# Kernel tuning notes

Hardware: AMD Instinct MI355X
Metric: run time of the kernel (lower is better)

The kernel has to match this reference:

```python
import jax, jax.numpy as jnp
import numpy as np
from jax import lax

B, C, L = 64, 768, 197
DEG = 3          # KACN Chebyshev degree
KW = 3           # conv kernel size
EPS = 1e-5       # BatchNorm eps
END_X = 14.0     # RoPE grid width (14x14 patch grid + 1 CLS token)


def _conv1d(x, W):
    # x: (B, Cin, L), W: (Cout, Cin, K); padding=1 keeps length
    return lax.conv_general_dilated(x, W, window_strides=(1,), padding=[(1, 1)],
                                    dimension_numbers=('NCH', 'OIH', 'NCH'))


def _batchnorm(y, scale, bias):
    # training-mode BatchNorm1d: biased stats over (batch, length)
    mean = jnp.mean(y, axis=(0, 2), keepdims=True)
    var = jnp.var(y, axis=(0, 2), keepdims=True)
    return (y - mean) * lax.rsqrt(var + EPS) * scale[None, :, None] + bias[None, :, None]


def _kacn_proj(x, W, scale, bias):
    # KACNConv1DLayer (groups=1): cos(arange(deg+1) * arccos(tanh(x))) basis, conv, BN
    b, c, l = x.shape
    z = jnp.arccos(jnp.tanh(x))[:, :, None, :] * jnp.arange(DEG + 1, dtype=x.dtype)[None, None, :, None]
    z = jnp.cos(z).reshape(b, c * (DEG + 1), l)  # (B, C*(DEG+1), L), channel-major pairing
    return _batchnorm(_conv1d(z, W), scale, bias)


def _rope(t, cosang, sinang):
    # rotate consecutive channel pairs; t: (B, N, C), cos/sin: (N, C//2)
    b, n, c = t.shape
    p = t.reshape(b, n, c // 2, 2)
    a, bb = p[..., 0], p[..., 1]
    ra = a * cosang[None] - bb * sinang[None]
    rb = a * sinang[None] + bb * cosang[None]
    return jnp.stack([ra, rb], axis=-1).reshape(b, n, c)


def reference(x, Wq, Wk, Wv, bnq_s, bnq_b, bnk_s, bnk_b, bnv_s, bnv_b, gamma, freqs, norm_s, norm_b):
    q = _kacn_proj(x, Wq, bnq_s, bnq_b)
    k = _kacn_proj(x, Wk, bnk_s, bnk_b)
    v = _kacn_proj(x, Wv, bnv_s, bnv_b)
    b, c, l = v.shape
    Q = q.transpose(0, 2, 1)  # (B, L, C)
    K = k.transpose(0, 2, 1)
    # mixed 2D RoPE angles (num_heads=1): t_x, t_y over 14x14 grid
    t = jnp.arange(l - 1, dtype=x.dtype)
    tx = jnp.mod(t, END_X)
    ty = jnp.floor(t / END_X)
    ang = tx[:, None] * freqs[0][None, :] + ty[:, None] * freqs[1][None, :]  # (L-1, C//2)
    cosang, sinang = jnp.cos(ang), jnp.sin(ang)
    # token 0 (CLS) is not rotated
    Qr = jnp.concatenate([Q[:, :1], _rope(Q[:, 1:], cosang, sinang)], axis=1)
    Kr = jnp.concatenate([K[:, :1], _rope(K[:, 1:], cosang, sinang)], axis=1)
    energy = jnp.einsum('bic,bjc->bij', Qr, Kr)          # unscaled, as in the module
    att = jax.nn.softmax(energy, axis=-1)
    out = jnp.einsum('bcj,bij->bci', v, att)             # v @ att^T
    return _batchnorm(gamma[0] * x + out, norm_s, norm_b)


def setup_inputs() -> dict:
    key = jax.random.key(0)
    ks = jax.random.split(key, 5)
    std = 1.0 / (C * (DEG + 1) * KW)
    x = jax.random.normal(ks[0], (B, C, L), dtype=jnp.float32)
    Wq = jax.random.normal(ks[1], (C, C * (DEG + 1), KW), dtype=jnp.float32) * std
    Wk = jax.random.normal(ks[2], (C, C * (DEG + 1), KW), dtype=jnp.float32) * std
    Wv = jax.random.normal(ks[3], (C, C * (DEG + 1), KW), dtype=jnp.float32) * std
    ones = jnp.ones((C,), jnp.float32)
    zeros = jnp.zeros((C,), jnp.float32)
    # init_2d_freqs(dim=C, num_heads=1, theta=10, rotate=True).view(2, -1)
    mag = 1.0 / 10.0 ** (np.arange(0, C, 4)[: C // 4].astype(np.float32) / C)
    ang = float(jax.random.uniform(ks[4], ())) * 2.0 * np.pi
    fx = np.concatenate([mag * np.cos(ang), mag * np.cos(np.pi / 2 + ang)])
    fy = np.concatenate([mag * np.sin(ang), mag * np.sin(np.pi / 2 + ang)])
    freqs = jnp.asarray(np.stack([fx, fy], axis=0), dtype=jnp.float32)  # (2, C//2)
    return {"x": x, "Wq": Wq, "Wk": Wk, "Wv": Wv,
            "bnq_s": ones, "bnq_b": zeros, "bnk_s": ones, "bnk_b": zeros,
            "bnv_s": ones, "bnv_b": zeros,
            "gamma": jnp.zeros((1,), jnp.float32), "freqs": freqs,
            "norm_s": ones, "norm_b": zeros}
```

## Files before the change

kernel.cpp:

```cpp
#include <hip/hip_runtime.h>

#define CCH 768
#define LL  197
#define L199 199
#define KC  2304
#define KTOT 6912
#define MK2 1769472
#define NVALID 12736
#define NROW 12608

typedef __bf16 bf16x8 __attribute__((ext_vector_type(8)));
typedef float f32x2 __attribute__((ext_vector_type(2)));
typedef float f32x4 __attribute__((ext_vector_type(4)));
typedef float f32x16 __attribute__((ext_vector_type(16)));

__device__ __forceinline__ unsigned short f2bf(float f) {
  unsigned int u = __float_as_uint(f);
  u += 0x7FFFu + ((u >> 16) & 1u);
  return (unsigned short)(u >> 16);
}
__device__ __forceinline__ float bf2f(unsigned short h) {
  return __uint_as_float(((unsigned int)h) << 16);
}

__global__ void pack_bias(const float* __restrict__ Wq, const float* __restrict__ Wk,
                          const float* __restrict__ Wv, unsigned short* __restrict__ Apack,
                          float* __restrict__ bias3, size_t pack1_halves) {
  __shared__ float wrow[9216];
  __shared__ float red0[256], red1[256], red2[256];
  const int bid = blockIdx.x;
  const int proj = bid / 768, m = bid % 768;
  const int t = threadIdx.x;
  const float* W = proj == 0 ? Wq : (proj == 1 ? Wk : Wv);
  const float* src = W + (size_t)m * 9216;
#pragma unroll
  for (int s = 0; s < 36; ++s) wrow[t + 256 * s] = src[t + 256 * s];
  __syncthreads();
  float s0 = 0.f, s1 = 0.f, s2 = 0.f;
  for (int c = t; c < 768; c += 256) {
    s0 += wrow[12 * c];
    s1 += wrow[12 * c + 1];
    s2 += wrow[12 * c + 2];
  }
  red0[t] = s0; red1[t] = s1; red2[t] = s2;
  unsigned short* Ahi = Apack + (size_t)proj * pack1_halves;
  unsigned short* Alo = Ahi + (size_t)768 * KTOT;
#pragma unroll
  for (int s = 0; s < 9; ++s) {
    int u = t + 256 * s;
    int c = u / 3, dm1 = u % 3;
    int ci = c * 4 + dm1 + 1;
#pragma unroll
    for (int tap = 0; tap < 3; ++tap) {
      float f = wrow[ci * 3 + tap];
      unsigned short hi = f2bf(f);
      unsigned short lo = f2bf(f - bf2f(hi));
      size_t idx = (size_t)m * KTOT + tap * KC + u;
      Ahi[idx] = hi;
      Alo[idx] = lo;
    }
  }
  __syncthreads();
  for (int off = 128; off; off >>= 1) {
    if (t < off) {
      red0[t] += red0[t + off];
      red1[t] += red1[t + off];
      red2[t] += red2[t + off];
    }
    __syncthreads();
  }
  if (t == 0) {
    bias3[proj * 2304 + m] = red0[0];
    bias3[proj * 2304 + 768 + m] = red1[0];
    bias3[proj * 2304 + 1536 + m] = red2[0];
  }
}

__global__ void z_kernel(const float* __restrict__ x, unsigned short* __restrict__ Zhi,
                         unsigned short* __restrict__ Zlo) {
  __shared__ float zs[3][32][33];
  int c0 = blockIdx.x * 32, l0 = blockIdx.y * 32, b = blockIdx.z;
  int t = threadIdx.x;
#pragma unroll
  for (int s = 0; s < 4; ++s) {
    int u = t + 256 * s;
    int rc = u >> 5, cl = u & 31;
    float v = 0.f;
    if (l0 + cl < LL) v = x[((size_t)b * CCH + c0 + rc) * LL + l0 + cl];
    float t1 = tanhf(v);
    zs[0][rc][cl] = t1;
    zs[1][rc][cl] = 2.f * t1 * t1 - 1.f;
    zs[2][rc][cl] = t1 * (4.f * t1 * t1 - 3.f);
  }
  __syncthreads();
#pragma unroll
  for (int s = 0; s < 12; ++s) {
    int w = t + 256 * s;
    int rl = w / 96, cc = w % 96;
    if (l0 + rl < LL) {
      int cl2 = cc / 3, dm1 = cc % 3;
      float v = zs[dm1][cl2][rl];
      unsigned short hi = f2bf(v);
      unsigned short lo = f2bf(v - bf2f(hi));
      size_t row = (size_t)b * L199 + 1 + l0 + rl;
      Zhi[row * KC + c0 * 3 + cc] = hi;
      Zlo[row * KC + c0 * 3 + cc] = lo;
    }
  }
}

__global__ void zero_zpad(unsigned short* __restrict__ Zhi, unsigned short* __restrict__ Zlo) {
  int u = blockIdx.x * 256 + threadIdx.x;
  if (u >= 132 * KC) return;
  int rowi = u / KC, c = u % KC;
  size_t r = (rowi < 128) ? ((size_t)(rowi >> 1) * L199 + (size_t)(rowi & 1) * 198)
                          : ((size_t)NVALID + rowi - 128);
  Zhi[r * KC + c] = 0;
  Zlo[r * KC + c] = 0;
}

#define GLL(SRC, DST) \
  __builtin_amdgcn_global_load_lds( \
      (const __attribute__((address_space(1))) void*)(SRC), \
      (__attribute__((address_space(3))) void*)(DST), 16, 0, 0)

__global__ __launch_bounds__(512, 2) void conv_gemm3(const unsigned short* __restrict__ Apack,
                                                     const unsigned short* __restrict__ Zhi,
                                                     const unsigned short* __restrict__ Zlo,
                                                     const float* __restrict__ bias3,
                                                     float* __restrict__ Oqk,
                                                     float* __restrict__ Ov) {
  __shared__ unsigned short lds[2 * 4 * 8192];
  const int bid = blockIdx.x;
  const int xcd = bid & 7, loc = bid >> 3;
  const int wg = (xcd < 2) ? (xcd * 57 + loc) : (114 + (xcd - 2) * 56 + loc);
  const int n_t = wg / 9, rem = wg % 9;
  const int proj = rem / 3, m_t = rem % 3;
  const int m_blk = m_t * 256, n_blk = n_t * 256;
  const unsigned short* Ahi = Apack + (size_t)proj * 2 * 768 * KTOT;
  const unsigned short* Alo = Ahi + (size_t)768 * KTOT;
  const float* bias3p = bias3 + proj * 2304;
  float* Op = (proj == 2) ? Ov : Oqk + (size_t)proj * NROW * CCH;

  const int t = threadIdx.x;
  const int wave = t >> 6, lane = t & 63;
  const int wm = (wave >> 2) * 128, wn = (wave & 3) * 64;
  f32x16 acc[4][2] = {};

  const int lt = ((lane >> 4) & 1) * 512 + (lane >> 5) * 128 + (lane & 15) * 8;
  const int auoff = (wm >> 4) * 512 + lt;
  const int buoff = (wn >> 4) * 512 + lt;

  const int prow = lane & 15;
  const int kch = lane >> 4;
  const unsigned short* srcs[8];
  int doff[8];
#pragma unroll
  for (int j = 0; j < 8; ++j) {
    int u = (wave << 3) + j;
    int tile = u >> 4, p = u & 15;
    doff[j] = tile * 8192 + p * 512;
    int r;
    const unsigned short* g;
    int rs;
    if (tile < 2) {
      r = m_blk + p * 16 + prow;
      g = (tile == 0) ? Ahi : Alo;
      rs = KTOT;
    } else {
      r = n_blk + p * 16 + prow;
      if (r > 12737) r = 12737;
      g = (tile == 2) ? Zhi : Zlo;
      rs = KC;
    }
    srcs[j] = g + (size_t)r * rs + kch * 8;
  }

  const int NIT = KTOT / 32;
#pragma unroll
  for (int j = 0; j < 8; ++j) GLL(srcs[j], lds + doff[j]);
#pragma unroll
  for (int j = 0; j < 6; ++j) GLL(srcs[j] + 32, lds + 32768 + doff[j]);
  asm volatile("s_waitcnt vmcnt(6)\n\ts_barrier" ::: "memory");
  __builtin_amdgcn_sched_barrier(0);

  for (int i = 0; i < NIT; ++i) {
    const unsigned short* lb = lds + ((i & 1) ? 32768 : 0);
    unsigned short* othbuf = lds + ((i & 1) ? 0 : 32768);
    unsigned short* curbuf = lds + ((i & 1) ? 32768 : 0);
    const int koff_prev = 32 * (i + 1);
    const int koff_cur  = 32 * (i + 2);
    const bool stage_prev = (i < NIT - 1);
    const bool stage_cur  = (i < NIT - 2);

    bf16x8 bh[2][2], bl[2][2];
    bf16x8 ah[2], al[2];

#pragma unroll
    for (int ks = 0; ks < 2; ++ks) {
#pragma unroll
      for (int nb = 0; nb < 2; ++nb) {
        bh[nb][ks] = *(const bf16x8*)(lb + 16384 + buoff + nb * 1024 + ks * 256);
        bl[nb][ks] = *(const bf16x8*)(lb + 24576 + buoff + nb * 1024 + ks * 256);
      }
      ah[ks] = *(const bf16x8*)(lb + auoff + ks * 256);
      al[ks] = *(const bf16x8*)(lb + 8192 + auoff + ks * 256);
    }
    if (stage_prev) {
      GLL(srcs[6] + koff_prev, othbuf + doff[6]);
      GLL(srcs[7] + koff_prev, othbuf + doff[7]);
    }
    asm volatile("s_barrier\n\ts_waitcnt lgkmcnt(0)" ::: "memory");
    __builtin_amdgcn_sched_barrier(0);
    __builtin_amdgcn_s_setprio(1);
#pragma unroll
    for (int p = 0; p < 3; ++p)
#pragma unroll
      for (int ks = 0; ks < 2; ++ks)
#pragma unroll
        for (int nb = 0; nb < 2; ++nb) {
          acc[0][nb] = __builtin_amdgcn_mfma_f32_32x32x16_bf16(
              p == 2 ? al[ks] : ah[ks], p == 1 ? bl[nb][ks] : bh[nb][ks], acc[0][nb], 0, 0, 0);
        }
    __builtin_amdgcn_s_setprio(0);
    asm volatile("s_barrier" ::: "memory");
    __builtin_amdgcn_sched_barrier(0);

#define PHASEQ(Q)                                                                 \
    {                                                                             \
      _Pragma("unroll") for (int ks = 0; ks < 2; ++ks) {                          \
        ah[ks] = *(const bf16x8*)(lb + auoff + (Q) * 1024 + ks * 256);            \
        al[ks] = *(const bf16x8*)(lb + 8192 + auoff + (Q) * 1024 + ks * 256);     \
      }                                                                           \
      if (stage_cur) {                                                            \
        GLL(srcs[2 * ((Q) - 1)] + koff_cur, curbuf + doff[2 * ((Q) - 1)]);        \
        GLL(srcs[2 * ((Q) - 1) + 1] + koff_cur, curbuf + doff[2 * ((Q) - 1) + 1]);\
      }                                                                           \
      asm volatile("s_barrier\n\ts_waitcnt lgkmcnt(0)" ::: "memory");             \
      __builtin_amdgcn_sched_barrier(0);                                          \
      __builtin_amdgcn_s_setprio(1);                                              \
      _Pragma("unroll") for (int p = 0; p < 3; ++p)                               \
      _Pragma("unroll") for (int ks = 0; ks < 2; ++ks)                            \
      _Pragma("unroll") for (int nb = 0; nb < 2; ++nb) {                          \
        acc[Q][nb] = __builtin_amdgcn_mfma_f32_32x32x16_bf16(                     \
            p == 2 ? al[ks] : ah[ks], p == 1 ? bl[nb][ks] : bh[nb][ks],           \
            acc[Q][nb], 0, 0, 0);                                                 \
      }                                                                           \
      __builtin_amdgcn_s_setprio(0);                                              \
    }

    PHASEQ(1)
    asm volatile("s_barrier" ::: "memory");
    __builtin_amdgcn_sched_barrier(0);
    PHASEQ(2)
    asm volatile("s_barrier" ::: "memory");
    __builtin_amdgcn_sched_barrier(0);
    PHASEQ(3)
    if (i < NIT - 2) {
      asm volatile("s_waitcnt vmcnt(6)\n\ts_barrier" ::: "memory");
    } else if (i == NIT - 2) {
      asm volatile("s_waitcnt vmcnt(0)\n\ts_barrier" ::: "memory");
    }
    __builtin_amdgcn_sched_barrier(0);
#undef PHASEQ
  }

  int rowarr[2];
  bool val[2], v0[2], v2[2];
#pragma unroll
  for (int nb = 0; nb < 2; ++nb) {
    int n = n_blk + wn + nb * 32 + (lane & 31);
    int b = n / L199, nl = n - b * L199;
    val[nb] = (n < NVALID) && (nl < LL);
    rowarr[nb] = b * LL + nl;
    v0[nb] = (nl == 0);
    v2[nb] = (nl == 196);
  }
#pragma unroll
  for (int mb = 0; mb < 4; ++mb) {
#pragma unroll
    for (int q = 0; q < 4; ++q) {
      int m = m_blk + wm + mb * 32 + q * 8 + (lane >> 5) * 4;
      f32x4 b0 = *(const f32x4*)(bias3p + m);
      f32x4 b1 = *(const f32x4*)(bias3p + 768 + m);
      f32x4 b2 = *(const f32x4*)(bias3p + 1536 + m);
      f32x4 bs = b0 + b1 + b2;
#pragma unroll
      for (int nb = 0; nb < 2; ++nb) {
        if (val[nb]) {
          f32x4 r;
          r[0] = acc[mb][nb][q * 4 + 0];
          r[1] = acc[mb][nb][q * 4 + 1];
          r[2] = acc[mb][nb][q * 4 + 2];
          r[3] = acc[mb][nb][q * 4 + 3];
          r += bs;
          if (v0[nb]) r -= b0;
          if (v2[nb]) r -= b2;
          *(f32x4*)(Op + (size_t)rowarr[nb] * CCH + m) = r;
        }
      }
    }
  }
}

__global__ void zero_f32(float* __restrict__ p, int n) {
  int u = blockIdx.x * 256 + threadIdx.x;
  if (u < n) p[u] = 0.f;
}

__global__ void bn_stats(const float* __restrict__ Oqk, const float* __restrict__ Ov,
                         float* __restrict__ Ssum, float* __restrict__ Ssq) {
  int proj = blockIdx.z;
  int cb = blockIdx.x * 64;
  int rb = blockIdx.y;
  int t = threadIdx.x;
  int ch = cb + (t & 63);
  int phase = t >> 6;
  const float* Op = (proj == 2) ? Ov : Oqk + (size_t)proj * NROW * CCH;
  float s = 0.f, q = 0.f;
  for (int r = rb * 394 + phase; r < rb * 394 + 394; r += 4) {
    float v = Op[(size_t)r * CCH + ch];
    s += v; q += v * v;
  }
  __shared__ float rs[256], rq[256];
  rs[t] = s; rq[t] = q;
  __syncthreads();
  if (t < 64) {
    float S = rs[t] + rs[t + 64] + rs[t + 128] + rs[t + 192];
    float Q = rq[t] + rq[t + 64] + rq[t + 128] + rq[t + 192];
    atomicAdd(&Ssum[proj * CCH + cb + t], S);
    atomicAdd(&Ssq[proj * CCH + cb + t], Q);
  }
}

__global__ void bn_fin(const float* __restrict__ Ssum, const float* __restrict__ Ssq,
                       const float* __restrict__ sq, const float* __restrict__ bq,
                       const float* __restrict__ sk, const float* __restrict__ bk,
                       const float* __restrict__ sv, const float* __restrict__ bv,
                       float* __restrict__ abn) {
  int u = blockIdx.x * 256 + threadIdx.x;
  if (u >= 3 * CCH) return;
  int proj = u / CCH, ch = u % CCH;
  float mean = Ssum[u] / 12608.f;
  float var = Ssq[u] / 12608.f - mean * mean;
  const float* sc = proj == 0 ? sq : (proj == 1 ? sk : sv);
  const float* bi = proj == 0 ? bq : (proj == 1 ? bk : bv);
  float a = sc[ch] * rsqrtf(var + 1e-5f);
  abn[u * 2] = a;
  abn[u * 2 + 1] = bi[ch] - mean * a;
}

__global__ void rope_pack(const float* __restrict__ Oqk, const float* __restrict__ abn,
                          const float* __restrict__ freqs, float* __restrict__ Qr,
                          float* __restrict__ Kr) {
  size_t u = (size_t)blockIdx.x * 256 + threadIdx.x;
  if (u >= 64ull * LL * 384) return;
  int c2 = (int)(u % 384);
  int l = (int)((u / 384) % LL);
  int b = (int)(u / (384ull * LL));
  size_t rowO = ((size_t)b * LL + l) * CCH + 2 * c2;
  const float* Ok = Oqk + (size_t)NROW * CCH;
  float q0 = Oqk[rowO], q1 = Oqk[rowO + 1];
  float k0 = Ok[rowO], k1 = Ok[rowO + 1];
  float aq0 = abn[(2 * c2) * 2],                bq0 = abn[(2 * c2) * 2 + 1];
  float aq1 = abn[(2 * c2 + 1) * 2],            bq1 = abn[(2 * c2 + 1) * 2 + 1];
  float ak0 = abn[(CCH + 2 * c2) * 2],          bk0 = abn[(CCH + 2 * c2) * 2 + 1];
  float ak1 = abn[(CCH + 2 * c2 + 1) * 2],      bk1 = abn[(CCH + 2 * c2 + 1) * 2 + 1];
  q0 = q0 * aq0 + bq0; q1 = q1 * aq1 + bq1;
  k0 = k0 * ak0 + bk0; k1 = k1 * ak1 + bk1;
  if (l > 0) {
    int tt = l - 1;
    float tx = (float)(tt % 14), ty = (float)(tt / 14);
    float ang = tx * freqs[c2] + ty * freqs[384 + c2];
    float sn, cs;
    sincosf(ang, &sn, &cs);
    float r0 = q0 * cs - q1 * sn, r1 = q0 * sn + q1 * cs;
    q0 = r0; q1 = r1;
    r0 = k0 * cs - k1 * sn; r1 = k0 * sn + k1 * cs;
    k0 = r0; k1 = r1;
  }
  size_t rowT = ((size_t)b * LL + l) * CCH + 2 * c2;
  Qr[rowT] = q0; Qr[rowT + 1] = q1;
  Kr[rowT] = k0; Kr[rowT + 1] = k1;
}

__global__ void energy_k(const float* __restrict__ Qr, const float* __restrict__ Kr,
                         float* __restrict__ E) {
  __shared__ float Qs[64][33], Ks[64][33];
  int i0 = blockIdx.x * 64, j0 = blockIdx.y * 64, b = blockIdx.z;
  int t = threadIdx.x, tj = t & 15, ti = t >> 4;
  float acc[4][4] = {};
  const float* Qb = Qr + (size_t)b * LL * CCH;
  const float* Kb = Kr + (size_t)b * LL * CCH;
  for (int k0 = 0; k0 < CCH; k0 += 32) {
    __syncthreads();
#pragma unroll
    for (int s = 0; s < 8; ++s) {
      int u = t + 256 * s, r = u >> 5, cc = u & 31;
      Qs[r][cc] = (i0 + r < LL) ? Qb[(size_t)(i0 + r) * CCH + k0 + cc] : 0.f;
      Ks[r][cc] = (j0 + r < LL) ? Kb[(size_t)(j0 + r) * CCH + k0 + cc] : 0.f;
    }
    __syncthreads();
#pragma unroll
    for (int kk = 0; kk < 32; ++kk) {
      float qv[4], kv[4];
#pragma unroll
      for (int q = 0; q < 4; ++q) qv[q] = Qs[ti * 4 + q][kk];
#pragma unroll
      for (int j = 0; j < 4; ++j) kv[j] = Ks[tj * 4 + j][kk];
#pragma unroll
      for (int q = 0; q < 4; ++q)
#pragma unroll
        for (int j = 0; j < 4; ++j) acc[q][j] += qv[q] * kv[j];
    }
  }
#pragma unroll
  for (int q = 0; q < 4; ++q) {
    int i = i0 + ti * 4 + q;
    if (i >= LL) continue;
#pragma unroll
    for (int j = 0; j < 4; ++j) {
      int jj = j0 + tj * 4 + j;
      if (jj < LL) E[((size_t)b * LL + i) * LL + jj] = acc[q][j];
    }
  }
}

__global__ void softmax_k(float* __restrict__ E) {
  int row = blockIdx.x;
  int lane = threadIdx.x;
  float* Er = E + (size_t)row * LL;
  float v[4];
  float m = -3.4e38f;
#pragma unroll
  for (int q = 0; q < 4; ++q) {
    int j = lane + 64 * q;
    v[q] = (j < LL) ? Er[j] : -3.4e38f;
    m = fmaxf(m, v[q]);
  }
  for (int off = 32; off; off >>= 1) m = fmaxf(m, __shfl_down(m, off));
  m = __shfl(m, 0);
  float s = 0.f;
#pragma unroll
  for (int q = 0; q < 4; ++q) {
    int j = lane + 64 * q;
    v[q] = (j < LL) ? expf(v[q] - m) : 0.f;
    s += v[q];
  }
  for (int off = 32; off; off >>= 1) s += __shfl_down(s, off);
  s = __shfl(s, 0);
  float inv = 1.f / s;
#pragma unroll
  for (int q = 0; q < 4; ++q) {
    int j = lane + 64 * q;
    if (j < LL) Er[j] = v[q] * inv;
  }
}

__global__ void av_y(const float* __restrict__ att, const float* __restrict__ Ov,
                     const float* __restrict__ abn, const float* __restrict__ x,
                     const float* __restrict__ gamma, float* __restrict__ Y) {
  __shared__ float As[32][33];
  __shared__ float Vs[32][128];
  __shared__ float Ts[32][129];
  int i0 = blockIdx.x * 32, c0 = blockIdx.y * 128, b = blockIdx.z;
  int t = threadIdx.x, tc = t & 63, tq = t >> 6;
  const float* attb = att + (size_t)b * LL * LL;
  float acc[8][2] = {};
  for (int j0 = 0; j0 < LL; j0 += 32) {
    __syncthreads();
#pragma unroll
    for (int s = 0; s < 4; ++s) {
      int u = t + 256 * s, r = u >> 5, cc = u & 31;
      As[r][cc] = (i0 + r < LL && j0 + cc < LL) ? attb[(size_t)(i0 + r) * LL + j0 + cc] : 0.f;
    }
#pragma unroll
    for (int s = 0; s < 16; ++s) {
      int u = t + 256 * s, r = u >> 7, cc = u & 127;
      Vs[r][cc] = (j0 + r < LL) ? Ov[((size_t)b * LL + j0 + r) * CCH + c0 + cc] : 0.f;
    }
    __syncthreads();
#pragma unroll
    for (int jj = 0; jj < 32; ++jj) {
      f32x2 vv = *(const f32x2*)&Vs[jj][2 * tc];
#pragma unroll
      for (int q = 0; q < 8; ++q) {
        float a = As[tq * 8 + q][jj];
        acc[q][0] += a * vv[0];
        acc[q][1] += a * vv[1];
      }
    }
  }
  int c = c0 + 2 * tc;
  float a0 = abn[(2 * CCH + c) * 2],     b0 = abn[(2 * CCH + c) * 2 + 1];
  float a1 = abn[(2 * CCH + c + 1) * 2], b1 = abn[(2 * CCH + c + 1) * 2 + 1];
#pragma unroll
  for (int q = 0; q < 8; ++q) {
    int il = tq * 8 + q;
    Ts[il][2 * tc] = a0 * acc[q][0] + b0;
    Ts[il][2 * tc + 1] = a1 * acc[q][1] + b1;
  }
  __syncthreads();
  float g = gamma[0];
#pragma unroll
  for (int s = 0; s < 16; ++s) {
    int u = t + 256 * s, cc = u >> 5, il = u & 31;
    if (i0 + il < LL) {
      size_t idx = ((size_t)b * CCH + c0 + cc) * LL + i0 + il;
      Y[idx] = g * x[idx] + Ts[il][cc];
    }
  }
}

__global__ void bn_y_final(const float* __restrict__ Y, const float* __restrict__ ns,
                           const float* __restrict__ nb, float* __restrict__ out) {
  __shared__ float ych[12608];
  __shared__ float rs[256], rq[256];
  int c = blockIdx.x;
  int t = threadIdx.x;
  float s = 0.f, q = 0.f;
  for (int u = t; u < 12608; u += 256) {
    int b = u / LL, l = u - b * LL;
    float v = Y[((size_t)b * CCH + c) * LL + l];
    ych[u] = v;
    s += v; q += v * v;
  }
  rs[t] = s; rq[t] = q;
  __syncthreads();
  for (int off = 128; off; off >>= 1) {
    if (t < off) { rs[t] += rs[t + off]; rq[t] += rq[t + off]; }
    __syncthreads();
  }
  float mean = rs[0] / 12608.f, var = rq[0] / 12608.f - mean * mean;
  float a = ns[c] * rsqrtf(var + 1e-5f);
  float bb = nb[c] - mean * a;
  for (int u = t; u < 12608; u += 256) {
    int b = u / LL, l = u - b * LL;
    out[((size_t)b * CCH + c) * LL + l] = a * ych[u] + bb;
  }
}

extern "C" void kernel_launch(void* const* d_in, const int* in_sizes, int n_in,
                              void* d_out, int out_size, void* d_ws, size_t ws_size,
                              hipStream_t stream) {
  const float* x = (const float*)d_in[0];
  const float* Wq = (const float*)d_in[1];
  const float* Wk = (const float*)d_in[2];
  const float* Wv = (const float*)d_in[3];
  const float* bnq_s = (const float*)d_in[4];
  const float* bnq_b = (const float*)d_in[5];
  const float* bnk_s = (const float*)d_in[6];
  const float* bnk_b = (const float*)d_in[7];
  const float* bnv_s = (const float*)d_in[8];
  const float* bnv_b = (const float*)d_in[9];
  const float* gamma = (const float*)d_in[10];
  const float* freqs = (const float*)d_in[11];
  const float* norm_s = (const float*)d_in[12];
  const float* norm_b = (const float*)d_in[13];
  float* out = (float*)d_out;

  char* ws = (char*)d_ws;
  const size_t QRSZ  = 38731776;
  const size_t PACK1 = 21233664;
  const size_t ZSZ   = 58705920;

  const size_t OFS_PACK = 0;
  const size_t OFS_Z    = 3 * PACK1;
  const size_t OFS_ZLO  = OFS_Z + ZSZ;
  const size_t OFS_O    = OFS_ZLO + ZSZ;
  const size_t OFS_MISC = OFS_O + 2 * QRSZ;

  unsigned short* Apack = (unsigned short*)(ws + OFS_PACK);
  unsigned short* Zhi = (unsigned short*)(ws + OFS_Z);
  unsigned short* Zlo = (unsigned short*)(ws + OFS_ZLO);
  float* Oqk = (float*)(ws + OFS_O);
  float* bias3 = (float*)(ws + OFS_MISC);
  float* Ssum = (float*)(ws + OFS_MISC + 27648);
  float* Ssq  = (float*)(ws + OFS_MISC + 36864);
  float* abn  = (float*)(ws + OFS_MISC + 46080);
  float* Ov = out;
  float* Qr = (float*)(ws + OFS_Z);
  float* Kr = (float*)(ws + OFS_Z + QRSZ);
  float* E  = (float*)(ws + OFS_Z + 2 * QRSZ);
  float* Y  = (float*)(ws + OFS_Z + QRSZ);

  zero_zpad<<<dim3((132 * KC + 255) / 256), 256, 0, stream>>>(Zhi, Zlo);
  z_kernel<<<dim3(24, 7, 64), 256, 0, stream>>>(x, Zhi, Zlo);
  pack_bias<<<dim3(2304), 256, 0, stream>>>(Wq, Wk, Wv, Apack, bias3, PACK1 / 2);
  conv_gemm3<<<dim3(450), 512, 0, stream>>>(Apack, Zhi, Zlo, bias3, Oqk, Ov);

  zero_f32<<<dim3(18), 256, 0, stream>>>(Ssum, 4608);
  bn_stats<<<dim3(12, 32, 3), 256, 0, stream>>>(Oqk, Ov, Ssum, Ssq);
  bn_fin<<<dim3(9), 256, 0, stream>>>(Ssum, Ssq, bnq_s, bnq_b, bnk_s, bnk_b, bnv_s, bnv_b, abn);
  rope_pack<<<dim3((unsigned)((64ull * LL * 384 + 255) / 256)), 256, 0, stream>>>(Oqk, abn, freqs, Qr, Kr);
  energy_k<<<dim3(4, 4, 64), 256, 0, stream>>>(Qr, Kr, E);
  softmax_k<<<dim3(64 * LL), 64, 0, stream>>>(E);
  av_y<<<dim3(7, 6, 64), 256, 0, stream>>>(E, Ov, abn, x, gamma, Y);
  bn_y_final<<<dim3(CCH), 256, 0, stream>>>(Y, norm_s, norm_b, out);
}
```

Measured before the change: 1.890 ms.

## Halve GEMM N-tile and K-step to raise occupancy and block count

Rewrites the conv GEMM main loop to use a 256x128 output tile with a K step of 16 instead of 256x256 with K step 32. This shrinks LDS to 48KB and the per-thread accumulators to 4 fragments, so launch bounds allow 4 blocks per CU, and the grid doubles to 900 blocks with a new XCD mapping. The intent is better occupancy and latency hiding. In exchange, each tile reuses less data (the A operand is loaded twice as often relative to compute) and there are twice as many barriers per unit of K.

```diff
diff --git a/kernel.cpp b/kernel.cpp
--- a/kernel.cpp
+++ b/kernel.cpp
@@ -124,19 +124,19 @@
       (const __attribute__((address_space(1))) void*)(SRC), \
       (__attribute__((address_space(3))) void*)(DST), 16, 0, 0)
 
-__global__ __launch_bounds__(512, 2) void conv_gemm3(const unsigned short* __restrict__ Apack,
+__global__ __launch_bounds__(512, 4) void conv_gemm3(const unsigned short* __restrict__ Apack,
                                                      const unsigned short* __restrict__ Zhi,
                                                      const unsigned short* __restrict__ Zlo,
                                                      const float* __restrict__ bias3,
                                                      float* __restrict__ Oqk,
                                                      float* __restrict__ Ov) {
-  __shared__ unsigned short lds[2 * 4 * 8192];
+  __shared__ unsigned short lds[2 * 12288];
   const int bid = blockIdx.x;
   const int xcd = bid & 7, loc = bid >> 3;
-  const int wg = (xcd < 2) ? (xcd * 57 + loc) : (114 + (xcd - 2) * 56 + loc);
+  const int wg = (xcd < 4) ? (xcd * 113 + loc) : (452 + (xcd - 4) * 112 + loc);
   const int n_t = wg / 9, rem = wg % 9;
   const int proj = rem / 3, m_t = rem % 3;
-  const int m_blk = m_t * 256, n_blk = n_t * 256;
+  const int m_blk = m_t * 256, n_blk = n_t * 128;
   const unsigned short* Ahi = Apack + (size_t)proj * 2 * 768 * KTOT;
   const unsigned short* Alo = Ahi + (size_t)768 * KTOT;
   const float* bias3p = bias3 + proj * 2304;
@@ -144,138 +144,108 @@
 
   const int t = threadIdx.x;
   const int wave = t >> 6, lane = t & 63;
-  const int wm = (wave >> 2) * 128, wn = (wave & 3) * 64;
-  f32x16 acc[4][2] = {};
-
-  const int lt = ((lane >> 4) & 1) * 512 + (lane >> 5) * 128 + (lane & 15) * 8;
-  const int auoff = (wm >> 4) * 512 + lt;
-  const int buoff = (wn >> 4) * 512 + lt;
-
-  const int prow = lane & 15;
-  const int kch = lane >> 4;
-  const unsigned short* srcs[8];
-  int doff[8];
-#pragma unroll
-  for (int j = 0; j < 8; ++j) {
-    int u = (wave << 3) + j;
-    int tile = u >> 4, p = u & 15;
-    doff[j] = tile * 8192 + p * 512;
-    int r;
-    const unsigned short* g;
-    int rs;
-    if (tile < 2) {
-      r = m_blk + p * 16 + prow;
-      g = (tile == 0) ? Ahi : Alo;
+  const int wm = (wave >> 2) * 128;
+  const int wn = (wave & 3) * 32;
+  const int g = wave >> 2;
+  const int fb = lane * 8;
+  const int aq = g * 2048;
+  const int bu = (wave & 3) * 512;
+  f32x16 acc[4] = {};
+
+  int uu[3];
+  uu[0] = 4 * (wave >> 1) + 2 + (wave & 1);
+  uu[1] = (wave < 4) ? 4 * wave : 2 * wave + 8;
+  uu[2] = (wave < 4) ? 4 * wave + 1 : 2 * wave + 9;
+  const unsigned short* srcs[3];
+  int doff[3];
+#pragma unroll
+  for (int j = 0; j < 3; ++j) {
+    int u = uu[j];
+    doff[j] = u * 512;
+    const unsigned short* gp;
+    int r, rs;
+    if (u < 16) {
+      int tile = u >> 3, p = u & 7;
+      r = m_blk + p * 32 + (lane & 31);
+      gp = tile ? Alo : Ahi;
       rs = KTOT;
     } else {
-      r = n_blk + p * 16 + prow;
+      int tile = (u - 16) >> 2, p = u & 3;
+      r = n_blk + p * 32 + (lane & 31);
       if (r > 12737) r = 12737;
-      g = (tile == 2) ? Zhi : Zlo;
+      gp = tile ? Zlo : Zhi;
       rs = KC;
     }
-    srcs[j] = g + (size_t)r * rs + kch * 8;
-  }
-
-  const int NIT = KTOT / 32;
-#pragma unroll
-  for (int j = 0; j < 8; ++j) GLL(srcs[j], lds + doff[j]);
-#pragma unroll
-  for (int j = 0; j < 6; ++j) GLL(srcs[j] + 32, lds + 32768 + doff[j]);
-  asm volatile("s_waitcnt vmcnt(6)\n\ts_barrier" ::: "memory");
+    srcs[j] = gp + (size_t)r * rs + (lane >> 5) * 8;
+  }
+
+  const int NIT = KTOT / 16;
+  GLL(srcs[0], lds + doff[0]);
+  GLL(srcs[1], lds + doff[1]);
+  GLL(srcs[2], lds + doff[2]);
+  GLL(srcs[2] + 16, lds + 12288 + doff[2]);
+  asm volatile("s_waitcnt vmcnt(1)\n\ts_barrier" ::: "memory");
   __builtin_amdgcn_sched_barrier(0);
 
   for (int i = 0; i < NIT; ++i) {
-    const unsigned short* lb = lds + ((i & 1) ? 32768 : 0);
-    unsigned short* othbuf = lds + ((i & 1) ? 0 : 32768);
-    unsigned short* curbuf = lds + ((i & 1) ? 32768 : 0);
-    const int koff_prev = 32 * (i + 1);
-    const int koff_cur  = 32 * (i + 2);
-    const bool stage_prev = (i < NIT - 1);
-    const bool stage_cur  = (i < NIT - 2);
-
-    bf16x8 bh[2][2], bl[2][2];
-    bf16x8 ah[2], al[2];
-
-#pragma unroll
-    for (int ks = 0; ks < 2; ++ks) {
-#pragma unroll
-      for (int nb = 0; nb < 2; ++nb) {
-        bh[nb][ks] = *(const bf16x8*)(lb + 16384 + buoff + nb * 1024 + ks * 256);
-        bl[nb][ks] = *(const bf16x8*)(lb + 24576 + buoff + nb * 1024 + ks * 256);
-      }
-      ah[ks] = *(const bf16x8*)(lb + auoff + ks * 256);
-      al[ks] = *(const bf16x8*)(lb + 8192 + auoff + ks * 256);
-    }
-    if (stage_prev) {
-      GLL(srcs[6] + koff_prev, othbuf + doff[6]);
-      GLL(srcs[7] + koff_prev, othbuf + doff[7]);
+    const unsigned short* lb = lds + ((i & 1) ? 12288 : 0);
+    unsigned short* oth = lds + ((i & 1) ? 0 : 12288);
+    unsigned short* cur = lds + ((i & 1) ? 12288 : 0);
+
+    bf16x8 bh = *(const bf16x8*)(lb + 8192 + bu + fb);
+    bf16x8 bl = *(const bf16x8*)(lb + 10240 + bu + fb);
+    bf16x8 a0h = *(const bf16x8*)(lb + aq + fb);
+    bf16x8 a0l = *(const bf16x8*)(lb + 4096 + aq + fb);
+    bf16x8 a1h = *(const bf16x8*)(lb + aq + 512 + fb);
+    bf16x8 a1l = *(const bf16x8*)(lb + 4096 + aq + 512 + fb);
+    if (i + 1 < NIT) {
+      const int ko = 16 * (i + 1);
+      GLL(srcs[0] + ko, oth + doff[0]);
+      GLL(srcs[1] + ko, oth + doff[1]);
     }
     asm volatile("s_barrier\n\ts_waitcnt lgkmcnt(0)" ::: "memory");
     __builtin_amdgcn_sched_barrier(0);
     __builtin_amdgcn_s_setprio(1);
-#pragma unroll
-    for (int p = 0; p < 3; ++p)
-#pragma unroll
-      for (int ks = 0; ks < 2; ++ks)
-#pragma unroll
-        for (int nb = 0; nb < 2; ++nb) {
-          acc[0][nb] = __builtin_amdgcn_mfma_f32_32x32x16_bf16(
-              p == 2 ? al[ks] : ah[ks], p == 1 ? bl[nb][ks] : bh[nb][ks], acc[0][nb], 0, 0, 0);
-        }
+    acc[0] = __builtin_amdgcn_mfma_f32_32x32x16_bf16(a0h, bh, acc[0], 0, 0, 0);
+    acc[0] = __builtin_amdgcn_mfma_f32_32x32x16_bf16(a0h, bl, acc[0], 0, 0, 0);
+    acc[0] = __builtin_amdgcn_mfma_f32_32x32x16_bf16(a0l, bh, acc[0], 0, 0, 0);
+    acc[1] = __builtin_amdgcn_mfma_f32_32x32x16_bf16(a1h, bh, acc[1], 0, 0, 0);
+    acc[1] = __builtin_amdgcn_mfma_f32_32x32x16_bf16(a1h, bl, acc[1], 0, 0, 0);
+    acc[1] = __builtin_amdgcn_mfma_f32_32x32x16_bf16(a1l, bh, acc[1], 0, 0, 0);
     __builtin_amdgcn_s_setprio(0);
     asm volatile("s_barrier" ::: "memory");
     __builtin_amdgcn_sched_barrier(0);
 
-#define PHASEQ(Q)                                                                 \
-    {                                                                             \
-      _Pragma("unroll") for (int ks = 0; ks < 2; ++ks) {                          \
-        ah[ks] = *(const bf16x8*)(lb + auoff + (Q) * 1024 + ks * 256);            \
-        al[ks] = *(const bf16x8*)(lb + 8192 + auoff + (Q) * 1024 + ks * 256);     \
-      }                                                                           \
-      if (stage_cur) {                                                            \
-        GLL(srcs[2 * ((Q) - 1)] + koff_cur, curbuf + doff[2 * ((Q) - 1)]);        \
-        GLL(srcs[2 * ((Q) - 1) + 1] + koff_cur, curbuf + doff[2 * ((Q) - 1) + 1]);\
-      }                                                                           \
-      asm volatile("s_barrier\n\ts_waitcnt lgkmcnt(0)" ::: "memory");             \
-      __builtin_amdgcn_sched_barrier(0);                                          \
-      __builtin_amdgcn_s_setprio(1);                                              \
-      _Pragma("unroll") for (int p = 0; p < 3; ++p)                               \
-      _Pragma("unroll") for (int ks = 0; ks < 2; ++ks)                            \
-      _Pragma("unroll") for (int nb = 0; nb < 2; ++nb) {                          \
-        acc[Q][nb] = __builtin_amdgcn_mfma_f32_32x32x16_bf16(                     \
-            p == 2 ? al[ks] : ah[ks], p == 1 ? bl[nb][ks] : bh[nb][ks],           \
-            acc[Q][nb], 0, 0, 0);                                                 \
-      }                                                                           \
-      __builtin_amdgcn_s_setprio(0);                                              \
-    }
-
-    PHASEQ(1)
-    asm volatile("s_barrier" ::: "memory");
+    bf16x8 a2h = *(const bf16x8*)(lb + aq + 1024 + fb);
+    bf16x8 a2l = *(const bf16x8*)(lb + 4096 + aq + 1024 + fb);
+    bf16x8 a3h = *(const bf16x8*)(lb + aq + 1536 + fb);
+    bf16x8 a3l = *(const bf16x8*)(lb + 4096 + aq + 1536 + fb);
+    if (i + 2 < NIT) {
+      GLL(srcs[2] + 16 * (i + 2), cur + doff[2]);
+    }
+    asm volatile("s_barrier\n\ts_waitcnt lgkmcnt(0)" ::: "memory");
     __builtin_amdgcn_sched_barrier(0);
-    PHASEQ(2)
-    asm volatile("s_barrier" ::: "memory");
-    __builtin_amdgcn_sched_barrier(0);
-    PHASEQ(3)
+    __builtin_amdgcn_s_setprio(1);
+    acc[2] = __builtin_amdgcn_mfma_f32_32x32x16_bf16(a2h, bh, acc[2], 0, 0, 0);
+    acc[2] = __builtin_amdgcn_mfma_f32_32x32x16_bf16(a2h, bl, acc[2], 0, 0, 0);
+    acc[2] = __builtin_amdgcn_mfma_f32_32x32x16_bf16(a2l, bh, acc[2], 0, 0, 0);
+    acc[3] = __builtin_amdgcn_mfma_f32_32x32x16_bf16(a3h, bh, acc[3], 0, 0, 0);
+    acc[3] = __builtin_amdgcn_mfma_f32_32x32x16_bf16(a3h, bl, acc[3], 0, 0, 0);
+    acc[3] = __builtin_amdgcn_mfma_f32_32x32x16_bf16(a3l, bh, acc[3], 0, 0, 0);
+    __builtin_amdgcn_s_setprio(0);
     if (i < NIT - 2) {
-      asm volatile("s_waitcnt vmcnt(6)\n\ts_barrier" ::: "memory");
+      asm volatile("s_waitcnt vmcnt(1)\n\ts_barrier" ::: "memory");
     } else if (i == NIT - 2) {
       asm volatile("s_waitcnt vmcnt(0)\n\ts_barrier" ::: "memory");
     }
     __builtin_amdgcn_sched_barrier(0);
-#undef PHASEQ
-  }
-
-  int rowarr[2];
-  bool val[2], v0[2], v2[2];
-#pragma unroll
-  for (int nb = 0; nb < 2; ++nb) {
-    int n = n_blk + wn + nb * 32 + (lane & 31);
-    int b = n / L199, nl = n - b * L199;
-    val[nb] = (n < NVALID) && (nl < LL);
-    rowarr[nb] = b * LL + nl;
-    v0[nb] = (nl == 0);
-    v2[nb] = (nl == 196);
-  }
+  }
+
+  int n = n_blk + wn + (lane & 31);
+  int nb_ = n / L199, nl = n - nb_ * L199;
+  bool val = (n < NVALID) && (nl < LL);
+  int row = nb_ * LL + nl;
+  bool v0 = (nl == 0), v2 = (nl == 196);
 #pragma unroll
   for (int mb = 0; mb < 4; ++mb) {
 #pragma unroll
@@ -285,19 +255,16 @@
       f32x4 b1 = *(const f32x4*)(bias3p + 768 + m);
       f32x4 b2 = *(const f32x4*)(bias3p + 1536 + m);
       f32x4 bs = b0 + b1 + b2;
-#pragma unroll
-      for (int nb = 0; nb < 2; ++nb) {
-        if (val[nb]) {
-          f32x4 r;
-          r[0] = acc[mb][nb][q * 4 + 0];
-          r[1] = acc[mb][nb][q * 4 + 1];
-          r[2] = acc[mb][nb][q * 4 + 2];
-          r[3] = acc[mb][nb][q * 4 + 3];
-          r += bs;
-          if (v0[nb]) r -= b0;
-          if (v2[nb]) r -= b2;
-          *(f32x4*)(Op + (size_t)rowarr[nb] * CCH + m) = r;
-        }
+      if (val) {
+        f32x4 r;
+        r[0] = acc[mb][q * 4 + 0];
+        r[1] = acc[mb][q * 4 + 1];
+        r[2] = acc[mb][q * 4 + 2];
+        r[3] = acc[mb][q * 4 + 3];
+        r += bs;
+        if (v0) r -= b0;
+        if (v2) r -= b2;
+        *(f32x4*)(Op + (size_t)row * CCH + m) = r;
       }
     }
   }
@@ -587,7 +554,7 @@
   zero_zpad<<<dim3((132 * KC + 255) / 256), 256, 0, stream>>>(Zhi, Zlo);
   z_kernel<<<dim3(24, 7, 64), 256, 0, stream>>>(x, Zhi, Zlo);
   pack_bias<<<dim3(2304), 256, 0, stream>>>(Wq, Wk, Wv, Apack, bias3, PACK1 / 2);
-  conv_gemm3<<<dim3(450), 512, 0, stream>>>(Apack, Zhi, Zlo, bias3, Oqk, Ov);
+  conv_gemm3<<<dim3(900), 512, 0, stream>>>(Apack, Zhi, Zlo, bias3, Oqk, Ov);
 
   zero_f32<<<dim3(18), 256, 0, stream>>>(Ssum, 4608);
   bn_stats<<<dim3(12, 32, 3), 256, 0, stream>>>(Oqk, Ov, Ssum, Ssq);
```

After: 2.522 ms. +33.5%, slower.
